# Optimization experiments

Hardware: AMD Instinct MI355X
Metric: run time of the kernel (lower is better)

The kernel has to match this reference:

```python
import jax, jax.numpy as jnp
import numpy as np
import math

NUM_HEADS = 16
HEAD_SIZE = 64
QKT_MEAN = 0.0
QKT_STD = 0.05
APPLY_NOISE = True
NOISE_KEY = jax.random.key(42)


def quantize_activation_8bit(x):
    max_abs = jnp.maximum(jnp.max(jnp.abs(x)), 1e-08)
    scale = max_abs / 127.0
    return jnp.clip(jnp.round(x / scale), -127, 127) * scale


def quantize_weight_4bit(w):
    max_abs = jnp.maximum(jnp.max(jnp.abs(w)), 1e-08)
    scale = max_abs / 7.0
    return jnp.clip(jnp.round(w / scale), -7, 7) * scale


def setup_inputs() -> dict:
    key = jax.random.key(0)
    k1, k2, k3, k4 = jax.random.split(key, 4)
    B, S, D = 4, 1024, 1024
    hidden_states = jax.random.normal(k1, (B, S, D), dtype=jnp.float32)
    attention_mask = jnp.zeros((B, 1, 1, S), dtype=jnp.float32)
    # nn.Linear weights are [out_features, in_features]
    w_scale = 1.0 / math.sqrt(D)
    Wq = jax.random.normal(k2, (D, D), dtype=jnp.float32) * w_scale
    Wk = jax.random.normal(k3, (D, D), dtype=jnp.float32) * w_scale
    Wv = jax.random.normal(k4, (D, D), dtype=jnp.float32) * w_scale
    return {"hidden_states": hidden_states, "attention_mask": attention_mask,
            "Wq": Wq, "Wk": Wk, "Wv": Wv}


def _split_heads(x):
    B, S, _ = x.shape
    return x.reshape(B, S, NUM_HEADS, HEAD_SIZE).transpose(0, 2, 1, 3)  # [B,H,S,Dh]


def reference(hidden_states, attention_mask, Wq, Wk, Wv):
    h_q = quantize_activation_8bit(hidden_states)
    h_k = quantize_activation_8bit(hidden_states)
    Q = _split_heads(jnp.einsum('bsd,od->bso', h_q, quantize_weight_4bit(Wq)))
    K = _split_heads(jnp.einsum('bsd,od->bso', h_k, quantize_weight_4bit(Wk)))
    V = _split_heads(jnp.einsum('bsd,od->bso', hidden_states, quantize_weight_4bit(Wv)))
    qkt = jnp.einsum('bhqd,bhkd->bhqk', Q, K) / math.sqrt(HEAD_SIZE)
    if APPLY_NOISE and QKT_STD > 0:
        noise = jax.random.normal(NOISE_KEY, qkt.shape, dtype=qkt.dtype) * QKT_STD + QKT_MEAN
        qkt = qkt + noise
    qkt = qkt + attention_mask  # [B,1,1,S] broadcasts over [B,H,S,S]
    attn_weights = jax.nn.softmax(qkt, axis=-1)  # dropout is identity in eval
    ctx = jnp.einsum('bhqk,bhkd->bhqd', attn_weights, V)
    B, H, S, Dh = ctx.shape
    ctx = ctx.transpose(0, 2, 1, 3).reshape(B, S, H * Dh)
    return ctx
```

## Files before the change

kernel.cpp:

```cpp
#include <hip/hip_runtime.h>
#include <hip/hip_bf16.h>

typedef unsigned short u16;
typedef unsigned int u32;
typedef __bf16 bf16x8 __attribute__((ext_vector_type(8)));
typedef __bf16 bf16x4 __attribute__((ext_vector_type(4)));
typedef float f32x4 __attribute__((ext_vector_type(4)));

#define MFMA16(a, b, c) __builtin_amdgcn_mfma_f32_16x16x32_bf16((a), (b), (c), 0, 0, 0)

static __device__ __forceinline__ u32 f2bfbits(float f) {
    union { float f; u32 u; } c; c.f = f;
    return (c.u + 0x7FFFu + ((c.u >> 16) & 1u)) >> 16;
}
static __device__ __forceinline__ u32 f2bfbits_exact(float f) {
    union { float f; u32 u; } c; c.f = f;
    return c.u >> 16;
}
static __device__ __forceinline__ u32 pack_bf16x2(float lo, float hi) {
    float2 v; v.x = lo; v.y = hi;
    union { __hip_bfloat162 h; u32 u; } c;
    c.h = __float22bfloat162_rn(v);
    return c.u;
}

static __device__ __forceinline__ u32 rotl_ab(u32 x, int r) {
    return __builtin_amdgcn_alignbit(x, x, 32 - r);
}

static __device__ __forceinline__ float exp2_fast(float x) {
    float r;
    asm("v_exp_f32 %0, %1\n\ts_nop 1" : "=v"(r) : "v"(x));
    return r;
}

static __device__ __forceinline__ void noise_pu8(u32 tk, float* __restrict__ pu) {
    const u32 K1 = 42u, K2 = 0x1BD11BF0u;
    u32 x0[8], x1[8];
#pragma unroll
    for (int d = 0; d < 8; d++) {
        u32 a = tk + (u32)(d < 4 ? d : 12 + d);
        x0[d] = a;
        x1[d] = rotl_ab(a, 13) ^ a;
    }
#define TFR(R)                                             \
    _Pragma("unroll") for (int d = 0; d < 8; d++) {        \
        x0[d] += x1[d];                                    \
        x1[d] = rotl_ab(x1[d], R) ^ x0[d];                 \
    }
#define TFRI(R, A, B)                                      \
    _Pragma("unroll") for (int d = 0; d < 8; d++) {        \
        x1[d] += (B);                                      \
        x0[d] += (A) + x1[d];              \
        x1[d] = rotl_ab(x1[d], R) ^ x0[d];                 \
    }
    TFR(15) TFR(26) TFR(6)
    TFRI(17, K1, K2 + 1u) TFR(29) TFR(16) TFR(24)
    TFRI(13, K2, 2u)      TFR(15) TFR(26) TFR(6)
    TFRI(17, 0u, K1 + 3u) TFR(29) TFR(16) TFR(24)
    TFRI(13, K1, K2 + 4u) TFR(15) TFR(26) TFR(6)
#undef TFR
#undef TFRI
#pragma unroll
    for (int d = 0; d < 8; d++) {
        u32 bits = (x0[d] + K2) ^ (x1[d] + 5u);
        float v2 = __uint_as_float((bits >> 9) | 0x40000000u);
        float u = v2 - 3.0f;
        float t = fmaf(-u, u, 1.0f);
        float L2 = __log2f(t);
        L2 = fmaxf(L2, -7.2134752f);
        float z = fmaf(L2, -0.69314718f, -2.5f);
        float p = 2.81022636e-08f;
        p = fmaf(p, z, 3.43273939e-07f);
        p = fmaf(p, z, -3.5233877e-06f);
        p = fmaf(p, z, -4.39150654e-06f);
        p = fmaf(p, z, 0.00021858087f);
        p = fmaf(p, z, -0.00125372503f);
        p = fmaf(p, z, -0.00417768164f);
        p = fmaf(p, z, 0.246640727f);
        p = fmaf(p, z, 1.50140941f);
        pu[d] = p * u;
    }
}

__global__ __launch_bounds__(256) void absmax_k(const float* __restrict__ h,
                                                const float* __restrict__ wq,
                                                const float* __restrict__ wk,
                                                const float* __restrict__ wv,
                                                u32* __restrict__ slots) {
    int t = blockIdx.y;
    const float* src = (t == 0) ? h : (t == 1) ? wq : (t == 2) ? wk : wv;
    int n4 = ((t == 0) ? 4096 * 1024 : 1024 * 1024) / 4;
    u32 mx = 0;
    int tid = threadIdx.x;
    for (int i = blockIdx.x * blockDim.x + tid; i < n4; i += gridDim.x * blockDim.x) {
        uint4 v = ((const uint4*)src)[i];
        mx = max(mx, v.x & 0x7FFFFFFFu);
        mx = max(mx, v.y & 0x7FFFFFFFu);
        mx = max(mx, v.z & 0x7FFFFFFFu);
        mx = max(mx, v.w & 0x7FFFFFFFu);
    }
    __shared__ u32 red[256];
    red[tid] = mx;
    __syncthreads();
    for (int s = 128; s > 0; s >>= 1) {
        if (tid < s) red[tid] = max(red[tid], red[tid + s]);
        __syncthreads();
    }
    if (tid == 0) atomicMax(&slots[t], red[0]);
}

__global__ __launch_bounds__(256) void prequant_all(const float* __restrict__ hidden,
                                                    const float* __restrict__ wq,
                                                    const float* __restrict__ wk,
                                                    const float* __restrict__ wv,
                                                    u16* __restrict__ hq,
                                                    u16* __restrict__ hbf,
                                                    u16* __restrict__ wqi,
                                                    u16* __restrict__ wki,
                                                    u16* __restrict__ wvi,
                                                    const u32* __restrict__ slots) {
    int y = blockIdx.y;
    const float* src = (y == 0) ? hidden : (y == 1) ? wq : (y == 2) ? wk : wv;
    u16* dqi = (y == 0) ? hq : (y == 1) ? wqi : (y == 2) ? wki : wvi;
    u16* draw = (y == 0) ? hbf : nullptr;
    float qmax = (y == 0) ? 127.0f : 7.0f;
    int n8 = ((y == 0) ? 4096 * 1024 : 1024 * 1024) / 8;

    float amax = fmaxf(__uint_as_float(slots[y]), 1e-8f);
    float scale = amax / qmax;
    for (int i = blockIdx.x * blockDim.x + threadIdx.x; i < n8; i += gridDim.x * blockDim.x) {
        float4 a = ((const float4*)src)[2 * i];
        float4 b = ((const float4*)src)[2 * i + 1];
        float x[8] = {a.x, a.y, a.z, a.w, b.x, b.y, b.z, b.w};
        u16 qi[8], rw[8];
#pragma unroll
        for (int j = 0; j < 8; j++) {
            float q = fminf(fmaxf(rintf(x[j] / scale), -qmax), qmax);
            qi[j] = (u16)f2bfbits_exact(q);
            rw[j] = (u16)f2bfbits(x[j]);
        }
        *(uint4*)(dqi + 8 * (size_t)i) = *(const uint4*)qi;
        if (draw) *(uint4*)(draw + 8 * (size_t)i) = *(const uint4*)rw;
    }
}

__global__ __launch_bounds__(256, 2) void qkv_gemm_all(const u16* __restrict__ hq,
                                                       const u16* __restrict__ hbf,
                                                       const u16* __restrict__ wqi,
                                                       const u16* __restrict__ wki,
                                                       const u16* __restrict__ wvi,
                                                       const u32* __restrict__ slots,
                                                       u16* __restrict__ Qb,
                                                       u16* __restrict__ Kb,
                                                       u16* __restrict__ Vtb) {
    __shared__ __align__(16) u16 As[128 * 40];
    __shared__ __align__(16) u16 Bs[128 * 40];
    int z = blockIdx.z;
    const u16* A  = (z < 2) ? hq : hbf;
    const u16* Bw = (z == 0) ? wqi : (z == 1) ? wki : wvi;
    u16* outp     = (z == 0) ? Qb : (z == 1) ? Kb : Vtb;
    int transOut = (z == 2);
    float s_a = fmaxf(__uint_as_float(slots[0]), 1e-8f) / 127.0f;
    float s_w = fmaxf(__uint_as_float(slots[z + 1]), 1e-8f) / 7.0f;
    float oscale = (z < 2) ? (s_a * s_w) : s_w;

    int tid = threadIdx.x;
    int srow = tid >> 2, scol = (tid & 3) * 8;
    int mbase = blockIdx.x * 128, nbase = blockIdx.y * 128;
    int lane = tid & 63, w = tid >> 6;
    int wv_m = w & 1, wv_n = w >> 1;
    int quad = lane >> 4, l16 = lane & 15;

    f32x4 acc[4][4];
#pragma unroll
    for (int i = 0; i < 4; i++)
#pragma unroll
        for (int j = 0; j < 4; j++) acc[i][j] = (f32x4){0.f, 0.f, 0.f, 0.f};

    const u16* aptr0 = A + (size_t)(mbase + srow) * 1024 + scol;
    const u16* aptr1 = A + (size_t)(mbase + 64 + srow) * 1024 + scol;
    const u16* bptr0 = Bw + (size_t)(nbase + srow) * 1024 + scol;
    const u16* bptr1 = Bw + (size_t)(nbase + 64 + srow) * 1024 + scol;

    for (int k0 = 0; k0 < 1024; k0 += 32) {
        uint4 a0 = *(const uint4*)(aptr0 + k0);
        uint4 a1 = *(const uint4*)(aptr1 + k0);
        uint4 b0 = *(const uint4*)(bptr0 + k0);
        uint4 b1 = *(const uint4*)(bptr1 + k0);
        __syncthreads();
        *(uint4*)(As + srow * 40 + scol) = a0;
        *(uint4*)(As + (64 + srow) * 40 + scol) = a1;
        *(uint4*)(Bs + srow * 40 + scol) = b0;
        *(uint4*)(Bs + (64 + srow) * 40 + scol) = b1;
        __syncthreads();
        bf16x8 af[4], bfr[4];
#pragma unroll
        for (int mt = 0; mt < 4; mt++)
            af[mt] = *(const bf16x8*)(As + (wv_m * 64 + mt * 16 + l16) * 40 + quad * 8);
#pragma unroll
        for (int nt = 0; nt < 4; nt++)
            bfr[nt] = *(const bf16x8*)(Bs + (wv_n * 64 + nt * 16 + l16) * 40 + quad * 8);
#pragma unroll
        for (int mt = 0; mt < 4; mt++)
#pragma unroll
            for (int nt = 0; nt < 4; nt++)
                acc[mt][nt] = MFMA16(af[mt], bfr[nt], acc[mt][nt]);
    }

#pragma unroll
    for (int mt = 0; mt < 4; mt++)
#pragma unroll
        for (int nt = 0; nt < 4; nt++)
#pragma unroll
            for (int r = 0; r < 4; r++) {
                float val = acc[mt][nt][r] * oscale;
                int m = mbase + wv_m * 64 + mt * 16 + quad * 4 + r;
                int o = nbase + wv_n * 64 + nt * 16 + l16;
                int b = m >> 10, s = m & 1023;
                int hh = o >> 6, dh = o & 63;
                size_t off = transOut ? (((size_t)(b * 16 + hh) * 64 + dh) * 1024 + s)
                                      : (((size_t)(b * 16 + hh) * 1024 + s) * 64 + dh);
                outp[off] = (u16)f2bfbits(val);
            }
}

struct KVTile {
    bf16x8 bk0, bk1, bk2, bk3;
    bf16x4 vlo[4], vhi[4];
};

static __device__ __forceinline__ void load_tile(KVTile& t,
                                                 const u16* __restrict__ Kb,
                                                 const u16* __restrict__ Vb,
                                                 int ks0, int kk, int l16, int quad) {
    const u16* Kt = Kb + (size_t)(ks0 + kk) * 64;
    t.bk0 = *(const bf16x8*)(Kt + l16 * 64 + quad * 8);
    t.bk1 = *(const bf16x8*)(Kt + l16 * 64 + 32 + quad * 8);
    t.bk2 = *(const bf16x8*)(Kt + (16 + l16) * 64 + quad * 8);
    t.bk3 = *(const bf16x8*)(Kt + (16 + l16) * 64 + 32 + quad * 8);
    const u16* Vk = Vb + kk + 4 * quad;
#pragma unroll
    for (int nt = 0; nt < 4; nt++) {
        t.vlo[nt] = *(const bf16x4*)(Vk + (nt * 16 + l16) * 1024);
        t.vhi[nt] = *(const bf16x4*)(Vk + (nt * 16 + l16) * 1024 + 16);
    }
}

static __device__ __forceinline__ void phase(const KVTile& t,
                                             f32x4 (&oacc)[4], f32x4& lacc,
                                             u32 tk, const float* __restrict__ maskb,
                                             int kk, int quad,
                                             bf16x8 aq0, bf16x8 aq1, bf16x8 ones) {
    const float IL2 = 1.4426950408889634f;
    const float C_S = 0.18033688011112042f;
    const float C_N = 0.10201394645f;

    f32x4 mk4 = *(const f32x4*)(maskb + kk + 4 * quad);
    f32x4 mh4 = *(const f32x4*)(maskb + kk + 16 + 4 * quad);
    mk4 = mk4 * IL2;
    mh4 = mh4 * IL2;

    float pu[8];
    noise_pu8(tk, pu);

    f32x4 s0 = (f32x4){0.f, 0.f, 0.f, 0.f};
    f32x4 s1 = (f32x4){0.f, 0.f, 0.f, 0.f};
    s0 = MFMA16(t.bk0, aq0, s0);
    s0 = MFMA16(t.bk1, aq1, s0);
    s1 = MFMA16(t.bk2, aq0, s1);
    s1 = MFMA16(t.bk3, aq1, s1);

    float e[8];
#pragma unroll
    for (int r = 0; r < 4; r++) {
        e[r]     = exp2_fast(fmaf(pu[r],     C_N, fmaf(s0[r], C_S, mk4[r])));
        e[4 + r] = exp2_fast(fmaf(pu[4 + r], C_N, fmaf(s1[r], C_S, mh4[r])));
    }
    union { u32 u[4]; bf16x8 v; } pf;
    pf.u[0] = pack_bf16x2(e[0], e[1]);
    pf.u[1] = pack_bf16x2(e[2], e[3]);
    pf.u[2] = pack_bf16x2(e[4], e[5]);
    pf.u[3] = pack_bf16x2(e[6], e[7]);

#pragma unroll
    for (int nt = 0; nt < 4; nt++) {
        bf16x8 vf = __builtin_shufflevector(t.vlo[nt], t.vhi[nt], 0, 1, 2, 3, 4, 5, 6, 7);
        oacc[nt] = MFMA16(pf.v, vf, oacc[nt]);
    }
    lacc = MFMA16(pf.v, ones, lacc);
}

__global__ __launch_bounds__(64, 4) void attn_kernel(const u16* __restrict__ Q,
                                                     const u16* __restrict__ K,
                                                     const u16* __restrict__ Vt,
                                                     const float* __restrict__ mask,
                                                     float* __restrict__ O0,
                                                     float* __restrict__ O1,
                                                     float* __restrict__ l0,
                                                     float* __restrict__ l1) {
    int qt = blockIdx.x, h = blockIdx.y;
    int b = blockIdx.z & 3, split = blockIdx.z >> 2;
    int bh = b * 16 + h;
    int lane = threadIdx.x & 63;
    int quad = lane >> 4, l16 = lane & 15;
    int q0 = qt * 16;
    int ks0 = split * 512;

    const float* maskb = mask + b * 1024 + ks0;

    float* Obuf = split ? O1 : O0;
    float* lbuf = split ? l1 : l0;
    const u16* Qb = Q + (size_t)bh * 1024 * 64;
    const u16* Kb = K + (size_t)bh * 1024 * 64;
    const u16* Vb = Vt + (size_t)bh * 64 * 1024 + ks0;

    bf16x8 aq0 = *(const bf16x8*)(Qb + (q0 + l16) * 64 + quad * 8);
    bf16x8 aq1 = *(const bf16x8*)(Qb + (q0 + l16) * 64 + 32 + quad * 8);

    union { u32 u[4]; bf16x8 v; } ones;
#pragma unroll
    for (int i = 0; i < 4; i++) ones.u[i] = 0x3F803F80u;

    f32x4 oacc[4];
#pragma unroll
    for (int i = 0; i < 4; i++) oacc[i] = (f32x4){0.f, 0.f, 0.f, 0.f};
    f32x4 lacc = (f32x4){0.f, 0.f, 0.f, 0.f};

    u32 tbase = ((u32)(bh * 1024 + q0 + l16)) * 1024u + (u32)ks0 + (u32)(4 * quad) + 42u;

    KVTile tA, tB;
    load_tile(tA, Kb, Vb, ks0, 0, l16, quad);

    for (int kk = 0; kk < 512; kk += 64) {
        load_tile(tB, Kb, Vb, ks0, kk + 32, l16, quad);
        phase(tA, oacc, lacc, tbase + (u32)kk, maskb, kk, quad, aq0, aq1, ones.v);
        if (kk + 64 < 512)
            load_tile(tA, Kb, Vb, ks0, kk + 64, l16, quad);
        phase(tB, oacc, lacc, tbase + (u32)(kk + 32), maskb, kk + 32, quad, aq0, aq1, ones.v);
    }

    if (l16 == 0) {
        int lbase = bh * 1024 + q0 + quad * 4;
#pragma unroll
        for (int r = 0; r < 4; r++) lbuf[lbase + r] = lacc[r];
    }
#pragma unroll
    for (int nt = 0; nt < 4; nt++) {
#pragma unroll
        for (int r = 0; r < 4; r++) {
            int q = q0 + quad * 4 + r;
            int dh = nt * 16 + l16;
            Obuf[((size_t)(b * 1024 + q)) * 1024 + h * 64 + dh] = oacc[nt][r];
        }
    }
}

__global__ __launch_bounds__(256) void combine_k(float* __restrict__ outp,
                                                 const float* __restrict__ O1,
                                                 const float* __restrict__ l0,
                                                 const float* __restrict__ l1) {
    int gid = blockIdx.x * 256 + threadIdx.x;
    int e = gid << 2;
    int bq = e >> 10;
    int h = (e & 1023) >> 6;
    int b = bq >> 10, q = bq & 1023;
    int lidx = ((b * 16 + h) << 10) + q;
    float linv = 1.0f / (l0[lidx] + l1[lidx]);
    float4 a = ((const float4*)outp)[gid];
    float4 c = ((const float4*)O1)[gid];
    float4 o;
    o.x = (a.x + c.x) * linv;
    o.y = (a.y + c.y) * linv;
    o.z = (a.z + c.z) * linv;
    o.w = (a.w + c.w) * linv;
    ((float4*)outp)[gid] = o;
}

extern "C" void kernel_launch(void* const* d_in, const int* in_sizes, int n_in,
                              void* d_out, int out_size, void* d_ws, size_t ws_size,
                              hipStream_t stream) {
    (void)in_sizes; (void)n_in; (void)out_size; (void)ws_size;
    const float* hidden = (const float*)d_in[0];
    const float* maskp  = (const float*)d_in[1];
    const float* Wq     = (const float*)d_in[2];
    const float* Wk     = (const float*)d_in[3];
    const float* Wv     = (const float*)d_in[4];
    float* outp = (float*)d_out;

    char* ws = (char*)d_ws;
    u32* slots = (u32*)ws;
    u16* hq  = (u16*)(ws + 256);
    u16* hbf = hq + 4096 * 1024;
    u16* wqi = hbf + 4096 * 1024;
    u16* wki = wqi + 1024 * 1024;
    u16* wvi = wki + 1024 * 1024;
    u16* Qb  = wvi + 1024 * 1024;
    u16* Kb  = Qb + 4096 * 1024;
    u16* Vtb = Kb + 4096 * 1024;

    float* O1buf = (float*)hq;
    float* l0buf = (float*)wqi;
    float* l1buf = l0buf + 4 * 16 * 1024;

    hipMemsetAsync(slots, 0, 16, stream);
    absmax_k<<<dim3(128, 4), 256, 0, stream>>>(hidden, Wq, Wk, Wv, slots);
    prequant_all<<<dim3(64, 4), 256, 0, stream>>>(hidden, Wq, Wk, Wv,
                                                  hq, hbf, wqi, wki, wvi, slots);
    qkv_gemm_all<<<dim3(32, 8, 3), 256, 0, stream>>>(hq, hbf, wqi, wki, wvi, slots,
                                                     Qb, Kb, Vtb);
    attn_kernel<<<dim3(64, 16, 8), 64, 0, stream>>>(Qb, Kb, Vtb, maskp,
                                                    outp, O1buf, l0buf, l1buf);
    combine_k<<<dim3(4096), 256, 0, stream>>>(outp, O1buf, l0buf, l1buf);
}
```

Measured before the change: 366.2 us.

## Use direct global-to-LDS loads in QKV GEMM and regroup attention into 4-wave blocks

The QKV GEMM now fills shared memory with global_load_lds 16-byte transfers instead of staging through registers, and drops the padded LDS row stride (40 to 32). The attention kernel packs four 16-row query tiles into one 256-thread block and removes the double-buffered K/V tile prefetch in favour of a simple load-then-compute loop. The RNG float conversion uses alignbit instead of a shift-or. Unpadded LDS rows may cause bank conflicts on the fragment reads, and losing the prefetch exposes load latency in attention.

```diff
diff --git a/kernel.cpp b/kernel.cpp
--- a/kernel.cpp
+++ b/kernel.cpp
@@ -8,6 +8,11 @@
 typedef float f32x4 __attribute__((ext_vector_type(4)));
 
 #define MFMA16(a, b, c) __builtin_amdgcn_mfma_f32_16x16x32_bf16((a), (b), (c), 0, 0, 0)
+
+#define GLOAD_LDS16(gp, lp)                                        \
+    __builtin_amdgcn_global_load_lds(                              \
+        (const __attribute__((address_space(1))) void*)(gp),       \
+        (__attribute__((address_space(3))) void*)(lp), 16, 0, 0)
 
 static __device__ __forceinline__ u32 f2bfbits(float f) {
     union { float f; u32 u; } c; c.f = f;
@@ -64,7 +69,8 @@
 #pragma unroll
     for (int d = 0; d < 8; d++) {
         u32 bits = (x0[d] + K2) ^ (x1[d] + 5u);
-        float v2 = __uint_as_float((bits >> 9) | 0x40000000u);
+        u32 vb = __builtin_amdgcn_alignbit(0x80u, bits, 9);
+        float v2 = __uint_as_float(vb);
         float u = v2 - 3.0f;
         float t = fmaf(-u, u, 1.0f);
         float L2 = __log2f(t);
@@ -154,8 +160,8 @@
                                                        u16* __restrict__ Qb,
                                                        u16* __restrict__ Kb,
                                                        u16* __restrict__ Vtb) {
-    __shared__ __align__(16) u16 As[128 * 40];
-    __shared__ __align__(16) u16 Bs[128 * 40];
+    __shared__ __align__(16) u16 As[128 * 32];
+    __shared__ __align__(16) u16 Bs[128 * 32];
     int z = blockIdx.z;
     const u16* A  = (z < 2) ? hq : hbf;
     const u16* Bw = (z == 0) ? wqi : (z == 1) ? wki : wvi;
@@ -166,41 +172,42 @@
     float oscale = (z < 2) ? (s_a * s_w) : s_w;
 
     int tid = threadIdx.x;
-    int srow = tid >> 2, scol = (tid & 3) * 8;
     int mbase = blockIdx.x * 128, nbase = blockIdx.y * 128;
     int lane = tid & 63, w = tid >> 6;
     int wv_m = w & 1, wv_n = w >> 1;
     int quad = lane >> 4, l16 = lane & 15;
 
+    int srow = lane >> 2, scol = (lane & 3) * 8;
+    const u16* ag0 = A + (size_t)(mbase + w * 32 + srow) * 1024 + scol;
+    const u16* ag1 = A + (size_t)(mbase + w * 32 + 16 + srow) * 1024 + scol;
+    const u16* bg0 = Bw + (size_t)(nbase + w * 32 + srow) * 1024 + scol;
+    const u16* bg1 = Bw + (size_t)(nbase + w * 32 + 16 + srow) * 1024 + scol;
+    u16* al0 = As + w * 1024;
+    u16* al1 = As + w * 1024 + 512;
+    u16* bl0 = Bs + w * 1024;
+    u16* bl1 = Bs + w * 1024 + 512;
+
     f32x4 acc[4][4];
 #pragma unroll
     for (int i = 0; i < 4; i++)
 #pragma unroll
         for (int j = 0; j < 4; j++) acc[i][j] = (f32x4){0.f, 0.f, 0.f, 0.f};
 
-    const u16* aptr0 = A + (size_t)(mbase + srow) * 1024 + scol;
-    const u16* aptr1 = A + (size_t)(mbase + 64 + srow) * 1024 + scol;
-    const u16* bptr0 = Bw + (size_t)(nbase + srow) * 1024 + scol;
-    const u16* bptr1 = Bw + (size_t)(nbase + 64 + srow) * 1024 + scol;
-
     for (int k0 = 0; k0 < 1024; k0 += 32) {
-        uint4 a0 = *(const uint4*)(aptr0 + k0);
-        uint4 a1 = *(const uint4*)(aptr1 + k0);
-        uint4 b0 = *(const uint4*)(bptr0 + k0);
-        uint4 b1 = *(const uint4*)(bptr1 + k0);
         __syncthreads();
-        *(uint4*)(As + srow * 40 + scol) = a0;
-        *(uint4*)(As + (64 + srow) * 40 + scol) = a1;
-        *(uint4*)(Bs + srow * 40 + scol) = b0;
-        *(uint4*)(Bs + (64 + srow) * 40 + scol) = b1;
+        GLOAD_LDS16(ag0 + k0, al0);
+        GLOAD_LDS16(ag1 + k0, al1);
+        GLOAD_LDS16(bg0 + k0, bl0);
+        GLOAD_LDS16(bg1 + k0, bl1);
         __syncthreads();
+
         bf16x8 af[4], bfr[4];
 #pragma unroll
         for (int mt = 0; mt < 4; mt++)
-            af[mt] = *(const bf16x8*)(As + (wv_m * 64 + mt * 16 + l16) * 40 + quad * 8);
+            af[mt] = *(const bf16x8*)(As + (wv_m * 64 + mt * 16 + l16) * 32 + quad * 8);
 #pragma unroll
         for (int nt = 0; nt < 4; nt++)
-            bfr[nt] = *(const bf16x8*)(Bs + (wv_n * 64 + nt * 16 + l16) * 40 + quad * 8);
+            bfr[nt] = *(const bf16x8*)(Bs + (wv_n * 64 + nt * 16 + l16) * 32 + quad * 8);
 #pragma unroll
         for (int mt = 0; mt < 4; mt++)
 #pragma unroll
@@ -291,20 +298,20 @@
     lacc = MFMA16(pf.v, ones, lacc);
 }
 
-__global__ __launch_bounds__(64, 4) void attn_kernel(const u16* __restrict__ Q,
-                                                     const u16* __restrict__ K,
-                                                     const u16* __restrict__ Vt,
-                                                     const float* __restrict__ mask,
-                                                     float* __restrict__ O0,
-                                                     float* __restrict__ O1,
-                                                     float* __restrict__ l0,
-                                                     float* __restrict__ l1) {
+__global__ __launch_bounds__(256, 4) void attn_kernel(const u16* __restrict__ Q,
+                                                      const u16* __restrict__ K,
+                                                      const u16* __restrict__ Vt,
+                                                      const float* __restrict__ mask,
+                                                      float* __restrict__ O0,
+                                                      float* __restrict__ O1,
+                                                      float* __restrict__ l0,
+                                                      float* __restrict__ l1) {
     int qt = blockIdx.x, h = blockIdx.y;
     int b = blockIdx.z & 3, split = blockIdx.z >> 2;
     int bh = b * 16 + h;
-    int lane = threadIdx.x & 63;
+    int tid = threadIdx.x, wv = tid >> 6, lane = tid & 63;
     int quad = lane >> 4, l16 = lane & 15;
-    int q0 = qt * 16;
+    int q0 = qt * 64 + wv * 16;
     int ks0 = split * 512;
 
     const float* maskb = mask + b * 1024 + ks0;
@@ -329,15 +336,10 @@
 
     u32 tbase = ((u32)(bh * 1024 + q0 + l16)) * 1024u + (u32)ks0 + (u32)(4 * quad) + 42u;
 
-    KVTile tA, tB;
-    load_tile(tA, Kb, Vb, ks0, 0, l16, quad);
-
-    for (int kk = 0; kk < 512; kk += 64) {
-        load_tile(tB, Kb, Vb, ks0, kk + 32, l16, quad);
-        phase(tA, oacc, lacc, tbase + (u32)kk, maskb, kk, quad, aq0, aq1, ones.v);
-        if (kk + 64 < 512)
-            load_tile(tA, Kb, Vb, ks0, kk + 64, l16, quad);
-        phase(tB, oacc, lacc, tbase + (u32)(kk + 32), maskb, kk + 32, quad, aq0, aq1, ones.v);
+    KVTile t;
+    for (int kk = 0; kk < 512; kk += 32) {
+        load_tile(t, Kb, Vb, ks0, kk, l16, quad);
+        phase(t, oacc, lacc, tbase + (u32)kk, maskb, kk, quad, aq0, aq1, ones.v);
     }
 
     if (l16 == 0) {
@@ -409,7 +411,7 @@
                                                   hq, hbf, wqi, wki, wvi, slots);
     qkv_gemm_all<<<dim3(32, 8, 3), 256, 0, stream>>>(hq, hbf, wqi, wki, wvi, slots,
                                                      Qb, Kb, Vtb);
-    attn_kernel<<<dim3(64, 16, 8), 64, 0, stream>>>(Qb, Kb, Vtb, maskp,
-                                                    outp, O1buf, l0buf, l1buf);
+    attn_kernel<<<dim3(16, 16, 8), 256, 0, stream>>>(Qb, Kb, Vtb, maskp,
+                                                     outp, O1buf, l0buf, l1buf);
     combine_k<<<dim3(4096), 256, 0, stream>>>(outp, O1buf, l0buf, l1buf);
 }
```

Result: faster. 355.4 us (-2.9%).
